# Kernel tuning notes

Measured on AMD Instinct MI355X. Metric: run time of the kernel, lower is better.

## Reference

```python
import jax, jax.numpy as jnp
import numpy as np

N = 50000      # nodes
E = 800000     # edges
F_IN = 128     # num_features
H = 64         # hidden_dim
G = 64         # graphs in batch
EPS = 1e-5


def setup_inputs() -> dict:
    ks = jax.random.split(jax.random.key(0), 16)
    x = jax.random.normal(ks[0], (N, F_IN), dtype=jnp.float32)
    edge_index = jax.random.randint(ks[1], (2, E), 0, N, dtype=jnp.int64)
    batch = jnp.sort(jax.random.randint(ks[2], (N,), 0, G, dtype=jnp.int64))
    s = 0.05
    inp = {"x": x, "edge_index": edge_index, "batch": batch}
    # GCNConv layers: W [out,in], bias [out]; BatchNorm gamma/beta [H]
    dims = [(H, F_IN), (H, H), (H, H)]
    for i, (o, ci) in enumerate(dims):
        inp[f"W{i}"] = jax.random.normal(ks[3 + i], (o, ci), dtype=jnp.float32) * s
        inp[f"b{i}"] = jnp.zeros((o,), dtype=jnp.float32)
        inp[f"g{i}"] = jnp.ones((o,), dtype=jnp.float32)
        inp[f"be{i}"] = jnp.zeros((o,), dtype=jnp.float32)
    inp["lin1_w"] = jax.random.normal(ks[10], (H // 2, H), dtype=jnp.float32) * s
    inp["lin1_b"] = jnp.zeros((H // 2,), dtype=jnp.float32)
    inp["lin2_w"] = jax.random.normal(ks[11], (1, H // 2), dtype=jnp.float32) * s
    inp["lin2_b"] = jnp.zeros((1,), dtype=jnp.float32)
    return inp


def _gcn_conv(x, src, dst, W, b):
    # PyG GCNConv: h = x W^T; add self-loops; symmetric deg^{-1/2} norm; scatter-add; + bias
    h = x @ W.T                                   # [N, out]
    n = x.shape[0]
    deg = jax.ops.segment_sum(jnp.ones(src.shape[0], h.dtype), dst, num_segments=n) + 1.0
    dinv = jax.lax.rsqrt(deg)                     # [N]
    msg = h[src] * (dinv[src] * dinv[dst])[:, None]   # per-edge messages
    agg = jax.ops.segment_sum(msg, dst, num_segments=n)
    agg = agg + h * (dinv * dinv)[:, None]        # self-loop contribution
    return agg + b


def _bn_relu(x, g, be):
    # BatchNorm1d (training-mode batch stats, biased var) + ReLU; dropout = identity (eval)
    m = x.mean(axis=0)
    v = jnp.var(x, axis=0)
    return jax.nn.relu((x - m) * jax.lax.rsqrt(v + EPS) * g + be)


def reference(x, edge_index, batch,
              W0, b0, g0, be0, W1, b1, g1, be1, W2, b2, g2, be2,
              lin1_w, lin1_b, lin2_w, lin2_b):
    src, dst = edge_index[0], edge_index[1]
    Ws = [(W0, b0, g0, be0), (W1, b1, g1, be1), (W2, b2, g2, be2)]
    h = x
    for (W, b, g, be) in Ws:
        h = _bn_relu(_gcn_conv(h, src, dst, W, b), g, be)
    # global mean pool over graphs
    sums = jax.ops.segment_sum(h, batch, num_segments=G)          # [G, H]
    cnt = jax.ops.segment_sum(jnp.ones((h.shape[0],), h.dtype), batch, num_segments=G)
    pooled = sums / jnp.maximum(cnt, 1.0)[:, None]
    h = jax.nn.relu(pooled @ lin1_w.T + lin1_b)
    return h @ lin2_w.T + lin2_b                                   # [G, 1]
```

## Files before the change

kernel.cpp:

```cpp
#include <hip/hip_runtime.h>

#define NN 50000
#define NE 800000
#define FIN 128
#define H 64
#define NG 64
#define BN_EPS 1e-5f
#define INV_N (1.0f / 50000.0f)
#define NBKT 196
#define PB 256
#define SLICE 64
#define BKCAP 8192
#define PROWS 16
#define NSEG 4

typedef float f4v __attribute__((ext_vector_type(4)));

__device__ __forceinline__ void f4acc(float4& a, const float4 b) {
    a.x += b.x; a.y += b.y; a.z += b.z; a.w += b.w;
}
__device__ __forceinline__ void f4accw(float4& a, const float4 b, float w) {
    a.x += b.x * w; a.y += b.y * w; a.z += b.z * w; a.w += b.w * w;
}
__device__ __forceinline__ void nt_store4(float* p, const float4 v) {
    __builtin_nontemporal_store(*(const f4v*)&v, (f4v*)p);
}

__global__ void prep(const float* __restrict__ W0, const float* __restrict__ W1,
                     const float* __restrict__ W2, const int* __restrict__ src,
                     const int* __restrict__ dst, float* __restrict__ Wt0,
                     float* __restrict__ Wt1, float* __restrict__ Wt2,
                     float* __restrict__ sl0, float* __restrict__ sl1,
                     float* __restrict__ sl2, float* __restrict__ pool,
                     float* __restrict__ cnt, int* __restrict__ cnts,
                     unsigned int* __restrict__ staged) {
    const int tid = threadIdx.x, bid = blockIdx.x;
    const int gtid = bid * 256 + tid;
    const int gsz = PB * 256;
    for (int i = gtid; i < 64 * 128; i += gsz) { sl0[i] = 0.f; sl1[i] = 0.f; sl2[i] = 0.f; }
    for (int i = gtid; i < NG * H; i += gsz) pool[i] = 0.f;
    if (gtid < NG) cnt[gtid] = 0.f;
    for (int i = gtid; i < FIN * 64; i += gsz) {
        int k = i >> 6, o = i & 63;
        Wt0[i] = W0[o * FIN + k];
    }
    for (int i = gtid; i < H * 64; i += gsz) {
        int k = i >> 6, o = i & 63;
        Wt1[i] = W1[o * H + k];
        Wt2[i] = W2[o * H + k];
    }
    __shared__ int hcnt[NBKT];
    for (int i = tid; i < NBKT; i += 256) hcnt[i] = 0;
    __syncthreads();
    const int chunk = NE / PB;
    const int e0 = bid * chunk, e1 = e0 + chunk;
    for (int e = e0 + tid; e < e1; e += 256) {
        int d = dst[e];
        int s = src[e];
        int bkt = d >> 8;
        int idx = atomicAdd(&hcnt[bkt], 1);
        if (idx < SLICE)
            staged[(size_t)(bkt * PB + bid) * SLICE + idx] =
                (unsigned int)s | ((unsigned int)(d & 255) << 16);
    }
    __syncthreads();
    for (int i = tid; i < NBKT; i += 256) cnts[i * PB + bid] = min(hcnt[i], SLICE);
}

union CsrMmSh {
    struct { float Xs[64 * 68]; float Ws[64 * 64]; } mm;
    struct { int cnt[256]; int loc[256]; int cur[256]; int spre[257]; } csr;
};

__device__ __forceinline__ int slice_find(const int* __restrict__ spre, int t) {
    int lo = 0, hi = 255;
    while (lo < hi) {
        int mid = (lo + hi + 1) >> 1;
        if (spre[mid] <= t) lo = mid; else hi = mid - 1;
    }
    return lo;
}

template <int K, bool SEGIN>
__device__ __forceinline__ void mm_tile_body(int base, const float* __restrict__ x,
                                             const float* __restrict__ Wtg,
                                             const float* __restrict__ slots,
                                             const float* __restrict__ gamma,
                                             const float* __restrict__ beta,
                                             const float* __restrict__ dv,
                                             float* __restrict__ outp, float* Xs, float* Ws,
                                             float* st, int n) {
    const int tid = threadIdx.x;
    if (slots) {
        if (tid < 128) {
            float s0 = 0.f, s1 = 0.f, s2 = 0.f, s3 = 0.f;
            for (int k = 0; k < 64; k += 4) {
                s0 += slots[(k + 0) * 128 + tid];
                s1 += slots[(k + 1) * 128 + tid];
                s2 += slots[(k + 2) * 128 + tid];
                s3 += slots[(k + 3) * 128 + tid];
            }
            st[tid] = (s0 + s1) + (s2 + s3);
        }
        __syncthreads();
    }
    const int q = tid >> 4;
    const int co = (tid & 15) * 4;
    const int kq = (tid & 15) * 4;
    float4 a0 = make_float4(0.f, 0.f, 0.f, 0.f);
    float4 a1 = a0, a2 = a0, a3 = a0;

    for (int kc = 0; kc < K; kc += 64) {
        if (kc) __syncthreads();
        for (int i = tid; i < 64 * 64; i += 256) Ws[i] = Wtg[kc * 64 + i];
        {
            const int kidx = kc + kq;
            float4 sc = make_float4(1.f, 1.f, 1.f, 1.f);
            float4 sh = make_float4(0.f, 0.f, 0.f, 0.f);
            if (slots) {
                float4 s = *(const float4*)&st[kidx];
                float4 ss = *(const float4*)&st[64 + kidx];
                float4 gm = *(const float4*)&gamma[kidx];
                float4 bt = *(const float4*)&beta[kidx];
                float mx = s.x * INV_N, my = s.y * INV_N, mz = s.z * INV_N, mw = s.w * INV_N;
                sc.x = gm.x * rsqrtf(ss.x * INV_N - mx * mx + BN_EPS);
                sc.y = gm.y * rsqrtf(ss.y * INV_N - my * my + BN_EPS);
                sc.z = gm.z * rsqrtf(ss.z * INV_N - mz * mz + BN_EPS);
                sc.w = gm.w * rsqrtf(ss.w * INV_N - mw * mw + BN_EPS);
                sh.x = bt.x - mx * sc.x;
                sh.y = bt.y - my * sc.y;
                sh.z = bt.z - mz * sc.z;
                sh.w = bt.w - mw * sc.w;
            }
            for (int j = 0; j < 4; ++j) {
                int r = (tid >> 4) + j * 16;
                int row = base + r;
                float4 v = make_float4(0.f, 0.f, 0.f, 0.f);
                if (row < n) {
                    if (SEGIN)
                        v = *(const float4*)&x[((size_t)(kidx >> 4) * NN + row) * 16 + (kidx & 15)];
                    else
                        v = *(const float4*)&x[(size_t)row * K + kidx];
                }
                if (slots) {
                    v.x = fmaxf(v.x * sc.x + sh.x, 0.f);
                    v.y = fmaxf(v.y * sc.y + sh.y, 0.f);
                    v.z = fmaxf(v.z * sc.z + sh.z, 0.f);
                    v.w = fmaxf(v.w * sc.w + sh.w, 0.f);
                }
                *(float4*)&Xs[r * 68 + kq] = v;
            }
        }
        __syncthreads();

#pragma unroll 2
        for (int k = 0; k < 64; k += 4) {
            float4 x0 = *(const float4*)&Xs[(q + 0) * 68 + k];
            float4 x1 = *(const float4*)&Xs[(q + 16) * 68 + k];
            float4 x2 = *(const float4*)&Xs[(q + 32) * 68 + k];
            float4 x3 = *(const float4*)&Xs[(q + 48) * 68 + k];
            float4 w0 = *(const float4*)&Ws[(k + 0) * 64 + co];
            float4 w1 = *(const float4*)&Ws[(k + 1) * 64 + co];
            float4 w2 = *(const float4*)&Ws[(k + 2) * 64 + co];
            float4 w3 = *(const float4*)&Ws[(k + 3) * 64 + co];

            a0.x += x0.x * w0.x + x0.y * w1.x + x0.z * w2.x + x0.w * w3.x;
            a0.y += x0.x * w0.y + x0.y * w1.y + x0.z * w2.y + x0.w * w3.y;
            a0.z += x0.x * w0.z + x0.y * w1.z + x0.z * w2.z + x0.w * w3.z;
            a0.w += x0.x * w0.w + x0.y * w1.w + x0.z * w2.w + x0.w * w3.w;

            a1.x += x1.x * w0.x + x1.y * w1.x + x1.z * w2.x + x1.w * w3.x;
            a1.y += x1.x * w0.y + x1.y * w1.y + x1.z * w2.y + x1.w * w3.y;
            a1.z += x1.x * w0.z + x1.y * w1.z + x1.z * w2.z + x1.w * w3.z;
            a1.w += x1.x * w0.w + x1.y * w1.w + x1.z * w2.w + x1.w * w3.w;

            a2.x += x2.x * w0.x + x2.y * w1.x + x2.z * w2.x + x2.w * w3.x;
            a2.y += x2.x * w0.y + x2.y * w1.y + x2.z * w2.y + x2.w * w3.y;
            a2.z += x2.x * w0.z + x2.y * w1.z + x2.z * w2.z + x2.w * w3.z;
            a2.w += x2.x * w0.w + x2.y * w1.w + x2.z * w2.w + x2.w * w3.w;

            a3.x += x3.x * w0.x + x3.y * w1.x + x3.z * w2.x + x3.w * w3.x;
            a3.y += x3.x * w0.y + x3.y * w1.y + x3.z * w2.y + x3.w * w3.y;
            a3.z += x3.x * w0.z + x3.y * w1.z + x3.z * w2.z + x3.w * w3.z;
            a3.w += x3.x * w0.w + x3.y * w1.w + x3.z * w2.w + x3.w * w3.w;
        }
    }

    const int sg = co >> 4, so = co & 15;
    int r0 = base + q;
    if (r0 < n) {
        float d = dv ? dv[r0] : 1.f;
        a0.x *= d; a0.y *= d; a0.z *= d; a0.w *= d;
        *(float4*)&outp[((size_t)sg * NN + r0) * 16 + so] = a0;
    }
    if (r0 + 16 < n) {
        float d = dv ? dv[r0 + 16] : 1.f;
        a1.x *= d; a1.y *= d; a1.z *= d; a1.w *= d;
        *(float4*)&outp[((size_t)sg * NN + r0 + 16) * 16 + so] = a1;
    }
    if (r0 + 32 < n) {
        float d = dv ? dv[r0 + 32] : 1.f;
        a2.x *= d; a2.y *= d; a2.z *= d; a2.w *= d;
        *(float4*)&outp[((size_t)sg * NN + r0 + 32) * 16 + so] = a2;
    }
    if (r0 + 48 < n) {
        float d = dv ? dv[r0 + 48] : 1.f;
        a3.x *= d; a3.y *= d; a3.z *= d; a3.w *= d;
        *(float4*)&outp[((size_t)sg * NN + r0 + 48) * 16 + so] = a3;
    }
}

__global__ __launch_bounds__(256, 4) void csr_mm0(
    const unsigned int* __restrict__ staged, const int* __restrict__ cnts,
    int* __restrict__ rs, int* __restrict__ re, float* __restrict__ dinv,
    unsigned short* __restrict__ csr, const float* __restrict__ x,
    const float* __restrict__ Wt0, float* __restrict__ bufA) {
    __shared__ CsrMmSh sh;
    const int tid = threadIdx.x;
    if (blockIdx.x < NBKT) {
        const int b = blockIdx.x;
        int c = cnts[b * PB + tid];
        sh.csr.loc[tid] = c;
        sh.csr.cnt[tid] = 0;
        __syncthreads();
        for (int off = 1; off < 256; off <<= 1) {
            int t = (tid >= off) ? sh.csr.loc[tid - off] : 0;
            __syncthreads();
            sh.csr.loc[tid] += t;
            __syncthreads();
        }
        sh.csr.spre[tid] = sh.csr.loc[tid] - c;
        if (tid == 255) sh.csr.spre[256] = sh.csr.loc[255];
        __syncthreads();
        const int T = sh.csr.spre[256];
        for (int t = tid; t < T; t += 256) {
            int s = slice_find(sh.csr.spre, t);
            unsigned int u = staged[(size_t)(b * PB + s) * SLICE + (t - sh.csr.spre[s])];
            atomicAdd(&sh.csr.cnt[(u >> 16) & 255], 1);
        }
        __syncthreads();
        int v = sh.csr.cnt[tid];
        sh.csr.loc[tid] = v;
        __syncthreads();
        for (int off = 1; off < 256; off <<= 1) {
            int t = (tid >= off) ? sh.csr.loc[tid - off] : 0;
            __syncthreads();
            sh.csr.loc[tid] += t;
            __syncthreads();
        }
        const int start = b * BKCAP + sh.csr.loc[tid] - v;
        const int node = b * 256 + tid;
        if (node < NN) {
            rs[node] = start;
            re[node] = start + v;
            dinv[node] = rsqrtf((float)v + 1.0f);
        }
        sh.csr.cur[tid] = start;
        __syncthreads();
        for (int t = tid; t < T; t += 256) {
            int s = slice_find(sh.csr.spre, t);
            unsigned int u = staged[(size_t)(b * PB + s) * SLICE + (t - sh.csr.spre[s])];
            int j = atomicAdd(&sh.csr.cur[(u >> 16) & 255], 1);
            csr[j] = (unsigned short)(u & 0xFFFFu);
        }
    } else {
        mm_tile_body<FIN, false>((blockIdx.x - NBKT) * 64, x, Wt0, nullptr, nullptr, nullptr,
                                 nullptr, bufA, sh.mm.Xs, sh.mm.Ws, nullptr, NN);
    }
}

__global__ __launch_bounds__(256, 4) void matmul_bn(const float* __restrict__ x,
                                                    const float* __restrict__ Wtg,
                                                    const float* __restrict__ slots,
                                                    const float* __restrict__ gamma,
                                                    const float* __restrict__ beta,
                                                    const float* __restrict__ dv,
                                                    float* __restrict__ outp, int n) {
    __shared__ float Xs[64 * 68];
    __shared__ float Ws[64 * 64];
    __shared__ __align__(16) float st[128];
    mm_tile_body<H, true>(blockIdx.x * 64, x, Wtg, slots, gamma, beta, dv, outp, Xs, Ws, st, n);
}

template <bool ED>
__global__ __launch_bounds__(256) void gather_seg4(const float* __restrict__ h,
                                                   const int* __restrict__ rs,
                                                   const int* __restrict__ re,
                                                   const unsigned short* __restrict__ csrc,
                                                   const float* __restrict__ dv,
                                                   const float* __restrict__ bias,
                                                   float* __restrict__ outp,
                                                   float* __restrict__ slots) {
    const int tid = threadIdx.x;
    const int bid = blockIdx.x;
    const int seg = bid & 3;
    const int wv = tid >> 6;
    const int lane = tid & 63;
    const int fl = lane & 3;
    const int ss = (lane >> 2) & 3;
    const int ds = lane >> 4;
    const int d = (bid >> 2) * 16 + wv * 4 + ds;
    const float* hseg = h + (size_t)seg * NN * 16;
    const int fo = fl * 4;
    const int j0 = __builtin_nontemporal_load(&rs[d]);
    const int j1 = __builtin_nontemporal_load(&re[d]);
    const float dA = dv[d];
    float4 acc = make_float4(0.f, 0.f, 0.f, 0.f);
    float4 acc2 = acc;
    int j = j0 + ss;
    while (j + 4 < j1) {
        int s0 = __builtin_nontemporal_load(&csrc[j]);
        int s1 = __builtin_nontemporal_load(&csrc[j + 4]);
        if (ED) {
            f4accw(acc, *(const float4*)&hseg[(size_t)s0 * 16 + fo], dv[s0]);
            f4accw(acc2, *(const float4*)&hseg[(size_t)s1 * 16 + fo], dv[s1]);
        } else {
            f4acc(acc, *(const float4*)&hseg[(size_t)s0 * 16 + fo]);
            f4acc(acc2, *(const float4*)&hseg[(size_t)s1 * 16 + fo]);
        }
        j += 8;
    }
    if (j < j1) {
        int s0 = __builtin_nontemporal_load(&csrc[j]);
        if (ED)
            f4accw(acc, *(const float4*)&hseg[(size_t)s0 * 16 + fo], dv[s0]);
        else
            f4acc(acc, *(const float4*)&hseg[(size_t)s0 * 16 + fo]);
    }
    f4acc(acc, acc2);
    acc.x += __shfl_xor(acc.x, 4); acc.x += __shfl_xor(acc.x, 8);
    acc.y += __shfl_xor(acc.y, 4); acc.y += __shfl_xor(acc.y, 8);
    acc.z += __shfl_xor(acc.z, 4); acc.z += __shfl_xor(acc.z, 8);
    acc.w += __shfl_xor(acc.w, 4); acc.w += __shfl_xor(acc.w, 8);
    const float4 self = *(const float4*)&hseg[(size_t)d * 16 + fo];
    const float4 bq = *(const float4*)&bias[seg * 16 + fo];
    const float sf = ED ? dA : 1.f;
    float4 v;
    v.x = bq.x + dA * (acc.x + sf * self.x);
    v.y = bq.y + dA * (acc.y + sf * self.y);
    v.z = bq.z + dA * (acc.z + sf * self.z);
    v.w = bq.w + dA * (acc.w + sf * self.w);
    if (ss == 0) nt_store4(&outp[((size_t)seg * NN + d) * 16 + fo], v);
    float4 q;
    q.x = v.x * v.x; q.y = v.y * v.y; q.z = v.z * v.z; q.w = v.w * v.w;
    v.x += __shfl_xor(v.x, 16); v.x += __shfl_xor(v.x, 32);
    v.y += __shfl_xor(v.y, 16); v.y += __shfl_xor(v.y, 32);
    v.z += __shfl_xor(v.z, 16); v.z += __shfl_xor(v.z, 32);
    v.w += __shfl_xor(v.w, 16); v.w += __shfl_xor(v.w, 32);
    q.x += __shfl_xor(q.x, 16); q.x += __shfl_xor(q.x, 32);
    q.y += __shfl_xor(q.y, 16); q.y += __shfl_xor(q.y, 32);
    q.z += __shfl_xor(q.z, 16); q.z += __shfl_xor(q.z, 32);
    q.w += __shfl_xor(q.w, 16); q.w += __shfl_xor(q.w, 32);
    __shared__ float4 red[2][4][4];
    if (ss == 0 && ds == 0) {
        red[0][wv][fl] = v;
        red[1][wv][fl] = q;
    }
    __syncthreads();
    if (tid < 8) {
        int a = tid >> 2, f = tid & 3;
        float4 s = red[a][0][f];
        f4acc(s, red[a][1][f]);
        f4acc(s, red[a][2][f]);
        f4acc(s, red[a][3][f]);
        float* slot = slots + ((bid >> 2) & 63) * 128 + a * 64 + seg * 16 + f * 4;
        atomicAdd(&slot[0], s.x);
        atomicAdd(&slot[1], s.y);
        atomicAdd(&slot[2], s.z);
        atomicAdd(&slot[3], s.w);
    }
}

__global__ void pool_seg(const float* __restrict__ h, const float* __restrict__ slots,
                         const float* __restrict__ gamma, const float* __restrict__ beta,
                         const int* __restrict__ batch, float* __restrict__ pool,
                         float* __restrict__ cnt, int n) {
    __shared__ __align__(16) float pst[128];
    if (threadIdx.x < 128) {
        float s0 = 0.f, s1 = 0.f, s2 = 0.f, s3 = 0.f;
        for (int k = 0; k < 64; k += 4) {
            s0 += slots[(k + 0) * 128 + threadIdx.x];
            s1 += slots[(k + 1) * 128 + threadIdx.x];
            s2 += slots[(k + 2) * 128 + threadIdx.x];
            s3 += slots[(k + 3) * 128 + threadIdx.x];
        }
        pst[threadIdx.x] = (s0 + s1) + (s2 + s3);
    }
    __syncthreads();
    int wave = blockIdx.x * 4 + (threadIdx.x >> 6);
    int c = threadIdx.x & 63;
    int r0 = wave * PROWS;
    if (r0 >= n) return;
    int r1 = min(r0 + PROWS, n);
    float mean = pst[c] * INV_N;
    float var = pst[64 + c] * INV_N - mean * mean;
    float sc = gamma[c] * rsqrtf(var + BN_EPS);
    float sh = beta[c] - mean * sc;
    const size_t segbase = (size_t)(c >> 4) * NN * 16 + (c & 15);
    int cur = batch[r0];
    float acc = 0.f;
    int nlocal = 0;
    for (int r = r0; r < r1; ++r) {
        int g = batch[r];
        if (g != cur) {
            atomicAdd(&pool[cur * H + c], acc);
            if (c == 0) atomicAdd(&cnt[cur], (float)nlocal);
            cur = g;
            acc = 0.f;
            nlocal = 0;
        }
        acc += fmaxf(h[segbase + (size_t)r * 16] * sc + sh, 0.f);
        ++nlocal;
    }
    atomicAdd(&pool[cur * H + c], acc);
    if (c == 0) atomicAdd(&cnt[cur], (float)nlocal);
}

__global__ void final_mlp(const float* __restrict__ pool, const float* __restrict__ cnt,
                          const float* __restrict__ l1w, const float* __restrict__ l1b,
                          const float* __restrict__ l2w, const float* __restrict__ l2b,
                          float* __restrict__ out) {
    int tid = blockIdx.x * 256 + threadIdx.x;
    int g = tid >> 5;
    int j = tid & 31;
    if (g >= NG) return;
    float inv = 1.0f / fmaxf(cnt[g], 1.0f);
    float s = l1b[j];
    for (int k = 0; k < H; ++k) s += pool[g * H + k] * inv * l1w[j * H + k];
    float v = fmaxf(s, 0.0f) * l2w[j];
    for (int off = 16; off > 0; off >>= 1) v += __shfl_down(v, off, 32);
    if (j == 0) out[g] = v + l2b[0];
}

extern "C" void kernel_launch(void* const* d_in, const int* in_sizes, int n_in,
                              void* d_out, int out_size, void* d_ws, size_t ws_size,
                              hipStream_t stream) {
    const float* x = (const float*)d_in[0];
    const int* ei = (const int*)d_in[1];
    const int* batch = (const int*)d_in[2];
    const float* W[3] = {(const float*)d_in[3], (const float*)d_in[7], (const float*)d_in[11]};
    const float* b[3] = {(const float*)d_in[4], (const float*)d_in[8], (const float*)d_in[12]};
    const float* g[3] = {(const float*)d_in[5], (const float*)d_in[9], (const float*)d_in[13]};
    const float* be[3] = {(const float*)d_in[6], (const float*)d_in[10], (const float*)d_in[14]};
    const float* l1w = (const float*)d_in[15];
    const float* l1b = (const float*)d_in[16];
    const float* l2w = (const float*)d_in[17];
    const float* l2b = (const float*)d_in[18];
    float* out = (float*)d_out;

    const int* src = ei;
    const int* dst = ei + NE;

    char* wsb = (char*)d_ws;
    size_t off = 0;
    auto alloc = [&](size_t elems) {
        void* p = wsb + off;
        off += elems * 4;
        return p;
    };
    float* dinv = (float*)alloc(50048);
    float* bufA = (float*)alloc((size_t)NN * H);
    float* bufB = (float*)alloc((size_t)NN * H);
    float* slots[3] = {(float*)alloc(64 * 128), (float*)alloc(64 * 128), (float*)alloc(64 * 128)};
    float* pool = (float*)alloc(NG * H);
    float* cnt = (float*)alloc(64);
    float* Wt[3] = {(float*)alloc(FIN * 64), (float*)alloc(H * 64), (float*)alloc(H * 64)};
    int* rs = (int*)alloc(50048);
    int* re = (int*)alloc(50048);
    int* cnts = (int*)alloc((size_t)NBKT * PB);
    unsigned int* staged = (unsigned int*)alloc((size_t)NBKT * PB * SLICE);
    unsigned short* csr = (unsigned short*)alloc((size_t)NBKT * BKCAP / 2);

    const int grid_mm = (NN + 63) / 64;
    const int grid_g4 = (NN / 16) * NSEG;

    prep<<<PB, 256, 0, stream>>>(W[0], W[1], W[2], src, dst, Wt[0], Wt[1], Wt[2], slots[0],
                                 slots[1], slots[2], pool, cnt, cnts, staged);
    csr_mm0<<<NBKT + grid_mm, 256, 0, stream>>>(staged, cnts, rs, re, dinv, csr, x, Wt[0], bufA);
    gather_seg4<true><<<grid_g4, 256, 0, stream>>>(bufA, rs, re, csr, dinv, b[0], bufB, slots[0]);
    matmul_bn<<<grid_mm, 256, 0, stream>>>(bufB, Wt[1], slots[0], g[0], be[0], dinv, bufA, NN);
    gather_seg4<false><<<grid_g4, 256, 0, stream>>>(bufA, rs, re, csr, dinv, b[1], bufB, slots[1]);
    matmul_bn<<<grid_mm, 256, 0, stream>>>(bufB, Wt[2], slots[1], g[1], be[1], dinv, bufA, NN);
    gather_seg4<false><<<grid_g4, 256, 0, stream>>>(bufA, rs, re, csr, dinv, b[2], bufB, slots[2]);
    const int pool_grid = ((NN + PROWS - 1) / PROWS + 3) / 4;
    pool_seg<<<pool_grid, 256, 0, stream>>>(bufB, slots[2], g[2], be[2], batch, pool, cnt, NN);
    final_mlp<<<8, 256, 0, stream>>>(pool, cnt, l1w, l1b, l2w, l2b, out);
}
```

Measured before the change: 357.1 us.

## Pad CSR rows to 8 and gather each node with one quad of lanes

The CSR build now rounds each node's row start up to a multiple of 8 entries. This lets the gather kernel read eight 16-bit source indices with one aligned 16-byte load. The gather kernel is remapped so each node is handled by 4 lanes instead of 16, 64 nodes per block. Each lane unrolls 8 neighbor loads per iteration into 4 accumulators, raising memory-level parallelism and removing the cross-lane edge-split reduction. The costs are fewer total threads, a serial tail loop on the long rows of high-degree nodes, and extra CSR space from padding within the fixed bucket capacity.

```diff
diff --git a/kernel.cpp b/kernel.cpp
--- a/kernel.cpp
+++ b/kernel.cpp
@@ -240,7 +240,8 @@
         }
         __syncthreads();
         int v = sh.csr.cnt[tid];
-        sh.csr.loc[tid] = v;
+        int vr = (v + 7) & ~7;
+        sh.csr.loc[tid] = vr;
         __syncthreads();
         for (int off = 1; off < 256; off <<= 1) {
             int t = (tid >= off) ? sh.csr.loc[tid - off] : 0;
@@ -248,7 +249,7 @@
             sh.csr.loc[tid] += t;
             __syncthreads();
         }
-        const int start = b * BKCAP + sh.csr.loc[tid] - v;
+        const int start = b * BKCAP + sh.csr.loc[tid] - vr;
         const int node = b * 256 + tid;
         if (node < NN) {
             rs[node] = start;
@@ -283,7 +284,7 @@
 }
 
 template <bool ED>
-__global__ __launch_bounds__(256) void gather_seg4(const float* __restrict__ h,
+__global__ __launch_bounds__(256) void gather_deep(const float* __restrict__ h,
                                                    const int* __restrict__ rs,
                                                    const int* __restrict__ re,
                                                    const unsigned short* __restrict__ csrc,
@@ -297,62 +298,83 @@
     const int wv = tid >> 6;
     const int lane = tid & 63;
     const int fl = lane & 3;
-    const int ss = (lane >> 2) & 3;
-    const int ds = lane >> 4;
-    const int d = (bid >> 2) * 16 + wv * 4 + ds;
+    const int ds = lane >> 2;
+    const int d = (bid >> 2) * 64 + wv * 16 + ds;
     const float* hseg = h + (size_t)seg * NN * 16;
     const int fo = fl * 4;
-    const int j0 = __builtin_nontemporal_load(&rs[d]);
-    const int j1 = __builtin_nontemporal_load(&re[d]);
-    const float dA = dv[d];
-    float4 acc = make_float4(0.f, 0.f, 0.f, 0.f);
-    float4 acc2 = acc;
-    int j = j0 + ss;
-    while (j + 4 < j1) {
-        int s0 = __builtin_nontemporal_load(&csrc[j]);
-        int s1 = __builtin_nontemporal_load(&csrc[j + 4]);
-        if (ED) {
-            f4accw(acc, *(const float4*)&hseg[(size_t)s0 * 16 + fo], dv[s0]);
-            f4accw(acc2, *(const float4*)&hseg[(size_t)s1 * 16 + fo], dv[s1]);
-        } else {
-            f4acc(acc, *(const float4*)&hseg[(size_t)s0 * 16 + fo]);
-            f4acc(acc2, *(const float4*)&hseg[(size_t)s1 * 16 + fo]);
-        }
-        j += 8;
-    }
-    if (j < j1) {
-        int s0 = __builtin_nontemporal_load(&csrc[j]);
-        if (ED)
-            f4accw(acc, *(const float4*)&hseg[(size_t)s0 * 16 + fo], dv[s0]);
-        else
-            f4acc(acc, *(const float4*)&hseg[(size_t)s0 * 16 + fo]);
-    }
-    f4acc(acc, acc2);
-    acc.x += __shfl_xor(acc.x, 4); acc.x += __shfl_xor(acc.x, 8);
-    acc.y += __shfl_xor(acc.y, 4); acc.y += __shfl_xor(acc.y, 8);
-    acc.z += __shfl_xor(acc.z, 4); acc.z += __shfl_xor(acc.z, 8);
-    acc.w += __shfl_xor(acc.w, 4); acc.w += __shfl_xor(acc.w, 8);
-    const float4 self = *(const float4*)&hseg[(size_t)d * 16 + fo];
-    const float4 bq = *(const float4*)&bias[seg * 16 + fo];
-    const float sf = ED ? dA : 1.f;
-    float4 v;
-    v.x = bq.x + dA * (acc.x + sf * self.x);
-    v.y = bq.y + dA * (acc.y + sf * self.y);
-    v.z = bq.z + dA * (acc.z + sf * self.z);
-    v.w = bq.w + dA * (acc.w + sf * self.w);
-    if (ss == 0) nt_store4(&outp[((size_t)seg * NN + d) * 16 + fo], v);
+    float4 v = make_float4(0.f, 0.f, 0.f, 0.f);
+    if (d < NN) {
+        const int j0 = __builtin_nontemporal_load(&rs[d]);
+        const int j1 = __builtin_nontemporal_load(&re[d]);
+        const float dA = dv[d];
+        float4 a0 = make_float4(0.f, 0.f, 0.f, 0.f), a1 = a0, a2 = a0, a3 = a0;
+        int j = j0;
+        while (j + 8 <= j1) {
+            int4 iv = *(const int4*)&csrc[j];
+            int s0 = iv.x & 0xFFFF, s1 = ((unsigned)iv.x) >> 16;
+            int s2 = iv.y & 0xFFFF, s3 = ((unsigned)iv.y) >> 16;
+            int s4 = iv.z & 0xFFFF, s5 = ((unsigned)iv.z) >> 16;
+            int s6 = iv.w & 0xFFFF, s7 = ((unsigned)iv.w) >> 16;
+            float4 t0 = *(const float4*)&hseg[(size_t)s0 * 16 + fo];
+            float4 t1 = *(const float4*)&hseg[(size_t)s1 * 16 + fo];
+            float4 t2 = *(const float4*)&hseg[(size_t)s2 * 16 + fo];
+            float4 t3 = *(const float4*)&hseg[(size_t)s3 * 16 + fo];
+            float4 t4 = *(const float4*)&hseg[(size_t)s4 * 16 + fo];
+            float4 t5 = *(const float4*)&hseg[(size_t)s5 * 16 + fo];
+            float4 t6 = *(const float4*)&hseg[(size_t)s6 * 16 + fo];
+            float4 t7 = *(const float4*)&hseg[(size_t)s7 * 16 + fo];
+            if (ED) {
+                float w0 = dv[s0], w1 = dv[s1], w2 = dv[s2], w3 = dv[s3];
+                float w4 = dv[s4], w5 = dv[s5], w6 = dv[s6], w7 = dv[s7];
+                f4accw(a0, t0, w0); f4accw(a1, t1, w1);
+                f4accw(a2, t2, w2); f4accw(a3, t3, w3);
+                f4accw(a0, t4, w4); f4accw(a1, t5, w5);
+                f4accw(a2, t6, w6); f4accw(a3, t7, w7);
+            } else {
+                f4acc(a0, t0); f4acc(a1, t1); f4acc(a2, t2); f4acc(a3, t3);
+                f4acc(a0, t4); f4acc(a1, t5); f4acc(a2, t6); f4acc(a3, t7);
+            }
+            j += 8;
+        }
+        for (; j < j1; ++j) {
+            int s = __builtin_nontemporal_load(&csrc[j]);
+            if (ED)
+                f4accw(a0, *(const float4*)&hseg[(size_t)s * 16 + fo], dv[s]);
+            else
+                f4acc(a0, *(const float4*)&hseg[(size_t)s * 16 + fo]);
+        }
+        f4acc(a0, a1);
+        f4acc(a2, a3);
+        f4acc(a0, a2);
+        const float4 self = *(const float4*)&hseg[(size_t)d * 16 + fo];
+        const float4 bq = *(const float4*)&bias[seg * 16 + fo];
+        const float sf = ED ? dA : 1.f;
+        v.x = bq.x + dA * (a0.x + sf * self.x);
+        v.y = bq.y + dA * (a0.y + sf * self.y);
+        v.z = bq.z + dA * (a0.z + sf * self.z);
+        v.w = bq.w + dA * (a0.w + sf * self.w);
+        nt_store4(&outp[((size_t)seg * NN + d) * 16 + fo], v);
+    }
     float4 q;
     q.x = v.x * v.x; q.y = v.y * v.y; q.z = v.z * v.z; q.w = v.w * v.w;
+    v.x += __shfl_xor(v.x, 4); v.x += __shfl_xor(v.x, 8);
     v.x += __shfl_xor(v.x, 16); v.x += __shfl_xor(v.x, 32);
+    v.y += __shfl_xor(v.y, 4); v.y += __shfl_xor(v.y, 8);
     v.y += __shfl_xor(v.y, 16); v.y += __shfl_xor(v.y, 32);
+    v.z += __shfl_xor(v.z, 4); v.z += __shfl_xor(v.z, 8);
     v.z += __shfl_xor(v.z, 16); v.z += __shfl_xor(v.z, 32);
+    v.w += __shfl_xor(v.w, 4); v.w += __shfl_xor(v.w, 8);
     v.w += __shfl_xor(v.w, 16); v.w += __shfl_xor(v.w, 32);
+    q.x += __shfl_xor(q.x, 4); q.x += __shfl_xor(q.x, 8);
     q.x += __shfl_xor(q.x, 16); q.x += __shfl_xor(q.x, 32);
+    q.y += __shfl_xor(q.y, 4); q.y += __shfl_xor(q.y, 8);
     q.y += __shfl_xor(q.y, 16); q.y += __shfl_xor(q.y, 32);
+    q.z += __shfl_xor(q.z, 4); q.z += __shfl_xor(q.z, 8);
     q.z += __shfl_xor(q.z, 16); q.z += __shfl_xor(q.z, 32);
+    q.w += __shfl_xor(q.w, 4); q.w += __shfl_xor(q.w, 8);
     q.w += __shfl_xor(q.w, 16); q.w += __shfl_xor(q.w, 32);
     __shared__ float4 red[2][4][4];
-    if (ss == 0 && ds == 0) {
+    if (ds == 0) {
         red[0][wv][fl] = v;
         red[1][wv][fl] = q;
     }
@@ -472,16 +494,16 @@
     unsigned short* csr = (unsigned short*)alloc((size_t)NBKT * BKCAP / 2);
 
     const int grid_mm = (NN + 63) / 64;
-    const int grid_g4 = (NN / 16) * NSEG;
+    const int grid_gd = grid_mm * NSEG;
 
     prep<<<PB, 256, 0, stream>>>(W[0], W[1], W[2], src, dst, Wt[0], Wt[1], Wt[2], slots[0],
                                  slots[1], slots[2], pool, cnt, cnts, staged);
     csr_mm0<<<NBKT + grid_mm, 256, 0, stream>>>(staged, cnts, rs, re, dinv, csr, x, Wt[0], bufA);
-    gather_seg4<true><<<grid_g4, 256, 0, stream>>>(bufA, rs, re, csr, dinv, b[0], bufB, slots[0]);
+    gather_deep<true><<<grid_gd, 256, 0, stream>>>(bufA, rs, re, csr, dinv, b[0], bufB, slots[0]);
     matmul_bn<<<grid_mm, 256, 0, stream>>>(bufB, Wt[1], slots[0], g[0], be[0], dinv, bufA, NN);
-    gather_seg4<false><<<grid_g4, 256, 0, stream>>>(bufA, rs, re, csr, dinv, b[1], bufB, slots[1]);
+    gather_deep<false><<<grid_gd, 256, 0, stream>>>(bufA, rs, re, csr, dinv, b[1], bufB, slots[1]);
     matmul_bn<<<grid_mm, 256, 0, stream>>>(bufB, Wt[2], slots[1], g[1], be[1], dinv, bufA, NN);
-    gather_seg4<false><<<grid_g4, 256, 0, stream>>>(bufA, rs, re, csr, dinv, b[2], bufB, slots[2]);
+    gather_deep<false><<<grid_gd, 256, 0, stream>>>(bufA, rs, re, csr, dinv, b[2], bufB, slots[2]);
     const int pool_grid = ((NN + PROWS - 1) / PROWS + 3) / 4;
     pool_seg<<<pool_grid, 256, 0, stream>>>(bufB, slots[2], g[2], be[2], batch, pool, cnt, NN);
     final_mlp<<<8, 256, 0, stream>>>(pool, cnt, l1w, l1b, l2w, l2b, out);
```

Result: faster. 317.1 us (-11.2%).
